# Kernel optimization log

Hardware: AMD Instinct MI355X
Metric: run time of the kernel (lower is better)

## Reference

```python
import jax, jax.numpy as jnp
from jax import lax
import numpy as np

H = 64
IN = 7
EPS = 1e-5


def _lstm_layer(x_seq, Wih, Whh, bih, bhh):
    # x_seq: [B, T, D] -> returns [B, T, H]; PyTorch gate order i,f,g,o
    B = x_seq.shape[0]
    b = bih + bhh
    x_tbd = jnp.swapaxes(x_seq, 0, 1)  # [T, B, D]
    # precompute input projections for all timesteps (one big GEMM)
    xproj = jnp.einsum('tbd,gd->tbg', x_tbd, Wih) + b  # [T, B, 4H]

    def step(carry, xp_t):
        h, c = carry
        gates = xp_t + h @ Whh.T  # [B, 4H]
        i, f, g, o = jnp.split(gates, 4, axis=-1)
        i = jax.nn.sigmoid(i)
        f = jax.nn.sigmoid(f)
        g = jnp.tanh(g)
        o = jax.nn.sigmoid(o)
        c = f * c + i * g
        h = o * jnp.tanh(c)
        return (h, c), h

    init = (jnp.zeros((B, H), x_seq.dtype), jnp.zeros((B, H), x_seq.dtype))
    _, hs = lax.scan(step, init, xproj)  # hs: [T, B, H]
    return jnp.swapaxes(hs, 0, 1)


def setup_inputs() -> dict:
    key = jax.random.key(0)
    ks = jax.random.split(key, 16)
    s = 1.0 / np.sqrt(H)
    u = lambda k, shape: jax.random.uniform(k, shape, jnp.float32, -s, s)
    inp = {
        'x': jax.random.normal(ks[0], (256, IN, 2048), jnp.float32),
        'Wih0': u(ks[1], (4 * H, IN)),
        'Whh0': u(ks[2], (4 * H, H)),
        'bih0': u(ks[3], (4 * H,)),
        'bhh0': u(ks[4], (4 * H,)),
        'Wih1': u(ks[5], (4 * H, H)),
        'Whh1': u(ks[6], (4 * H, H)),
        'bih1': u(ks[7], (4 * H,)),
        'bhh1': u(ks[8], (4 * H,)),
        'W1': u(ks[9], (10, H)),
        'b1': u(ks[10], (10,)),
        'gamma': jnp.ones((10,), jnp.float32),
        'beta': jnp.zeros((10,), jnp.float32),
        'rm': jax.random.normal(ks[11], (10,), jnp.float32) * 0.1,
        'rv': jax.random.uniform(ks[12], (10,), jnp.float32, 0.5, 1.5),
        'W2': u(ks[13], (1, 10)),
        'b2': u(ks[14], (1,)),
    }
    return inp


def reference(x, Wih0, Whh0, bih0, bhh0, Wih1, Whh1, bih1, bhh1,
              W1, b1, gamma, beta, rm, rv, W2, b2):
    # x: [B, 7, T] -> permute to [B, T, 7] (batch_first LSTM input)
    xs = jnp.transpose(x, (0, 2, 1))
    h0 = _lstm_layer(xs, Wih0, Whh0, bih0, bhh0)   # [B, T, H]
    h1 = _lstm_layer(h0, Wih1, Whh1, bih1, bhh1)   # [B, T, H] (dropout=0.05 inactive in eval)
    last = h1[:, -1, :]                            # [B, H]
    y = last @ W1.T + b1                           # [B, 10]
    y = (y - rm) * lax.rsqrt(rv + EPS) * gamma + beta  # BN1d eval mode
    y = jax.nn.relu(y)
    return y @ W2.T + b2                           # [B, 1]
```

## Files before the change

### kernel.cpp

```cpp
#include <hip/hip_runtime.h>
#include <math.h>

#define HH  64
#define TT  2048
#define IND 7
#define NT  256

typedef _Float16 half_t;
typedef _Float16 h2v __attribute__((ext_vector_type(2)));
typedef _Float16 h8v __attribute__((ext_vector_type(8)));
typedef unsigned int u2v __attribute__((ext_vector_type(2)));

#define LOG2E 1.44269504088896f

#define S2C(V, I) __builtin_shufflevector(V, V, 2*(I), 2*(I)+1)

__device__ __forceinline__ float fdot2(h2v a, h2v b, float c) {
#if __has_builtin(__builtin_amdgcn_fdot2)
    return __builtin_amdgcn_fdot2(a, b, c, false);
#else
    return fmaf((float)a.x, (float)b.x, fmaf((float)a.y, (float)b.y, c));
#endif
}

__device__ __forceinline__ float exp2_fast(float x) {
#if __has_builtin(__builtin_amdgcn_exp2f)
    return __builtin_amdgcn_exp2f(x);
#else
    return exp2f(x);
#endif
}
__device__ __forceinline__ float rcp_fast(float x) {
#if __has_builtin(__builtin_amdgcn_rcpf)
    return __builtin_amdgcn_rcpf(x);
#else
    return __fdividef(1.0f, x);
#endif
}

__device__ __forceinline__ float partner32(float x, int kh) {
#if __has_builtin(__builtin_amdgcn_permlane32_swap)
    u2v r = __builtin_amdgcn_permlane32_swap(__float_as_uint(x), __float_as_uint(x), false, false);
    return kh ? __uint_as_float(r.x) : __uint_as_float(r.y);
#else
    return __shfl_xor(x, 32);
#endif
}

__device__ __forceinline__ float sig2(float ahat) {
    return rcp_fast(1.0f + exp2_fast(-ahat));
}
__device__ __forceinline__ float tanh2(float c) {
    float e = exp2_fast(c * (-2.0f * LOG2E));
    return fmaf(2.0f, rcp_fast(1.0f + e), -1.0f);
}

#define DOT4(ACC, W, H) \
    ACC = fdot2((W)[0], S2C(H, 0), ACC); \
    ACC = fdot2((W)[1], S2C(H, 1), ACC); \
    ACC = fdot2((W)[2], S2C(H, 2), ACC); \
    ACC = fdot2((W)[3], S2C(H, 3), ACC);

__global__ __launch_bounds__(NT) __attribute__((amdgpu_waves_per_eu(1, 1)))
void lstm2_fused(
    const float* __restrict__ x,
    const float* __restrict__ Wih0,
    const float* __restrict__ Whh0,
    const float* __restrict__ bih0, const float* __restrict__ bhh0,
    const float* __restrict__ Wih1,
    const float* __restrict__ Whh1,
    const float* __restrict__ bih1, const float* __restrict__ bhh1,
    const float* __restrict__ W1,
    const float* __restrict__ b1v,
    const float* __restrict__ gmma, const float* __restrict__ beta,
    const float* __restrict__ rm,   const float* __restrict__ rv,
    const float* __restrict__ W2,
    const float* __restrict__ b2,
    float* __restrict__ out)
{
    const int b    = blockIdx.x;
    const int tid  = threadIdx.x;
    const int wave = tid >> 6;
    const int lane = tid & 63;
    const int kh   = lane >> 5;
    const int j    = ((wave & 1) << 5) | (lane & 31);
    const bool pub = (kh == 0);

    __shared__ __align__(16) half_t xTh[TT][8];
    __shared__ __align__(16) half_t h0r[4][HH];
    __shared__ __align__(16) half_t h1r[2][HH];
    __shared__ float yv[10];

    {
        const float* xg = x + (size_t)b * (IND * TT);
        for (int i = tid; i < IND * TT; i += NT) {
            int d = i >> 11;
            int t = i & (TT - 1);
            xTh[t][d] = (half_t)xg[i];
        }
        for (int t = tid; t < TT; t += NT) xTh[t][7] = (half_t)0.0f;
        if (tid < HH) {
            h0r[3][tid] = (half_t)0.0f;
            h1r[1][tid] = (half_t)0.0f;
        }
    }

    __syncthreads();

    if (wave < 2) {
        h2v wh[4][16];
        h2v xw[4][4];
        float bg[4];
        #pragma unroll
        for (int s = 0; s < 4; ++s) {
            const int g = (s << 6) | j;
            const float sc = (s == 2) ? 2.0f * LOG2E : LOG2E;
            const float* pw = Whh0 + g * HH + 32 * kh;
            #pragma unroll
            for (int r = 0; r < 16; ++r)
                wh[s][r] = h2v{(half_t)(pw[2*r] * sc), (half_t)(pw[2*r+1] * sc)};
            float t8[8];
            #pragma unroll
            for (int d = 0; d < 8; ++d)
                t8[d] = (d < IND && kh) ? Wih0[g * IND + d] * sc : 0.0f;
            #pragma unroll
            for (int r = 0; r < 4; ++r)
                xw[s][r] = h2v{(half_t)t8[2*r], (half_t)t8[2*r+1]};
            bg[s] = (kh == 0) ? (bih0[g] + bhh0[g]) * sc : 0.0f;
        }

        float c0 = 0.0f;
        h8v XV = *((const h8v*)&xTh[0][0]);

        for (int tick = 0; tick <= TT + 1; ++tick) {
            if (tick < TT) {
                const h8v* hp = (const h8v*)&h0r[(tick - 1) & 3][32 * kh];
                h8v H0 = hp[0], H1 = hp[1], H2 = hp[2], H3 = hp[3];
                float fr[4];
                #pragma unroll
                for (int s = 0; s < 4; ++s) {
                    float a0 = bg[s], a1 = 0.f, a2 = 0.f, a3 = 0.f;
                    DOT4(a0, &xw[s][0], XV)
                    DOT4(a0, &wh[s][0],  H0)
                    DOT4(a1, &wh[s][4],  H1)
                    DOT4(a2, &wh[s][8],  H2)
                    DOT4(a3, &wh[s][12], H3)
                    fr[s] = (a0 + a1) + (a2 + a3);
                }
                float fi = fr[0] + partner32(fr[0], kh);
                float ff = fr[1] + partner32(fr[1], kh);
                float fg = fr[2] + partner32(fr[2], kh);
                float fo = fr[3] + partner32(fr[3], kh);
                float iv = sig2(fi);
                float fv = sig2(ff);
                float gv = fmaf(2.0f, sig2(fg), -1.0f);
                float ov = sig2(fo);
                c0 = fmaf(fv, c0, iv * gv);
                float hn = ov * tanh2(c0);
                if (pub) h0r[tick & 3][j] = (half_t)hn;
                XV = *((const h8v*)&xTh[(tick + 1) & (TT - 1)][0]);
            }
            __syncthreads();
        }
    } else {
        h2v wi[4][16], wh[4][16];
        float bg[4];
        #pragma unroll
        for (int s = 0; s < 4; ++s) {
            const int g = (s << 6) | j;
            const float sc = (s == 2) ? 2.0f * LOG2E : LOG2E;
            const float* p0 = Wih1 + g * HH + 32 * kh;
            const float* p1 = Whh1 + g * HH + 32 * kh;
            #pragma unroll
            for (int r = 0; r < 16; ++r) {
                wi[s][r] = h2v{(half_t)(p0[2*r] * sc), (half_t)(p0[2*r+1] * sc)};
                wh[s][r] = h2v{(half_t)(p1[2*r] * sc), (half_t)(p1[2*r+1] * sc)};
            }
            bg[s] = (kh == 0) ? (bih1[g] + bhh1[g]) * sc : 0.0f;
        }

        float c1 = 0.0f;
        h8v P0 = {}, P1 = {}, P2 = {}, P3 = {};

        for (int tick = 0; tick <= TT + 1; ++tick) {
            if (tick >= 2) {
                const h8v* q = (const h8v*)&h1r[(tick - 3) & 1][32 * kh];
                h8v Q0 = q[0], Q1 = q[1], Q2 = q[2], Q3 = q[3];
                float fr[4];
                #pragma unroll
                for (int s = 0; s < 4; ++s) {
                    float a0 = bg[s], a1 = 0.f, a2 = 0.f, a3 = 0.f;
                    DOT4(a0, &wi[s][0],  P0)
                    DOT4(a1, &wi[s][4],  P1)
                    DOT4(a2, &wi[s][8],  P2)
                    DOT4(a3, &wi[s][12], P3)
                    DOT4(a0, &wh[s][0],  Q0)
                    DOT4(a1, &wh[s][4],  Q1)
                    DOT4(a2, &wh[s][8],  Q2)
                    DOT4(a3, &wh[s][12], Q3)
                    fr[s] = (a0 + a1) + (a2 + a3);
                }
                float fi = fr[0] + partner32(fr[0], kh);
                float ff = fr[1] + partner32(fr[1], kh);
                float fg = fr[2] + partner32(fr[2], kh);
                float fo = fr[3] + partner32(fr[3], kh);
                float iv = sig2(fi);
                float fv = sig2(ff);
                float gv = fmaf(2.0f, sig2(fg), -1.0f);
                float ov = sig2(fo);
                c1 = fmaf(fv, c1, iv * gv);
                float hn = ov * tanh2(c1);
                if (pub) h1r[tick & 1][j] = (half_t)hn;
            }
            if (tick >= 1) {
                const h8v* pp = (const h8v*)&h0r[(tick - 1) & 3][32 * kh];
                P0 = pp[0]; P1 = pp[1]; P2 = pp[2]; P3 = pp[3];
            }
            __syncthreads();
        }
    }

    if (tid < 10) {
        float y = b1v[tid];
        #pragma unroll
        for (int k = 0; k < HH; ++k) y += W1[tid * HH + k] * (float)h1r[1][k];
        y = (y - rm[tid]) * rsqrtf(rv[tid] + 1e-5f) * gmma[tid] + beta[tid];
        y = fmaxf(y, 0.0f);
        yv[tid] = y * W2[tid];
    }
    __syncthreads();
    if (tid == 0) {
        float sacc = b2[0];
        #pragma unroll
        for (int k = 0; k < 10; ++k) sacc += yv[k];
        out[b] = sacc;
    }
}

extern "C" void kernel_launch(void* const* d_in, const int* in_sizes, int n_in,
                              void* d_out, int out_size, void* d_ws, size_t ws_size,
                              hipStream_t stream) {
    const float* x    = (const float*)d_in[0];
    const float* Wih0 = (const float*)d_in[1];
    const float* Whh0 = (const float*)d_in[2];
    const float* bih0 = (const float*)d_in[3];
    const float* bhh0 = (const float*)d_in[4];
    const float* Wih1 = (const float*)d_in[5];
    const float* Whh1 = (const float*)d_in[6];
    const float* bih1 = (const float*)d_in[7];
    const float* bhh1 = (const float*)d_in[8];
    const float* W1   = (const float*)d_in[9];
    const float* b1   = (const float*)d_in[10];
    const float* gmma = (const float*)d_in[11];
    const float* beta = (const float*)d_in[12];
    const float* rm   = (const float*)d_in[13];
    const float* rv   = (const float*)d_in[14];
    const float* W2   = (const float*)d_in[15];
    const float* b2   = (const float*)d_in[16];

    const int B = in_sizes[0] / (IND * TT);

    lstm2_fused<<<dim3(B), dim3(NT), 0, stream>>>(
        x, Wih0, Whh0, bih0, bhh0, Wih1, Whh1, bih1, bhh1,
        W1, b1, gmma, beta, rm, rv, W2, b2, (float*)d_out);
}
```

Baseline: 1.040 ms.

## Offload LSTM input projections to dedicated producer waves via shared memory

Adds two more waves (384 threads) that compute the layer-0 input projection from x and the layer-1 input projection from layer-0 h. Both results go through double-buffered shared arrays, one tick ahead of the recurrent waves that consume them. The layer-0 and layer-1 recurrent waves then only do the hidden-to-hidden dot products on their serial per-timestep path, which halves layer-1 arithmetic per step. The cost is extra shared-memory traffic, a deeper pipeline and a barrier across six waves instead of four each step.

```diff
diff --git a/kernel.cpp b/kernel.cpp
--- a/kernel.cpp
+++ b/kernel.cpp
@@ -4,11 +4,12 @@
 #define HH  64
 #define TT  2048
 #define IND 7
-#define NT  256
+#define NT  384
 
 typedef _Float16 half_t;
 typedef _Float16 h2v __attribute__((ext_vector_type(2)));
 typedef _Float16 h8v __attribute__((ext_vector_type(8)));
+typedef float    f4v __attribute__((ext_vector_type(4)));
 typedef unsigned int u2v __attribute__((ext_vector_type(2)));
 
 #define LOG2E 1.44269504088896f
@@ -61,7 +62,7 @@
     ACC = fdot2((W)[2], S2C(H, 2), ACC); \
     ACC = fdot2((W)[3], S2C(H, 3), ACC);
 
-__global__ __launch_bounds__(NT) __attribute__((amdgpu_waves_per_eu(1, 1)))
+__global__ __launch_bounds__(NT) __attribute__((amdgpu_waves_per_eu(1, 2)))
 void lstm2_fused(
     const float* __restrict__ x,
     const float* __restrict__ Wih0,
@@ -89,6 +90,8 @@
     __shared__ __align__(16) half_t xTh[TT][8];
     __shared__ __align__(16) half_t h0r[4][HH];
     __shared__ __align__(16) half_t h1r[2][HH];
+    __shared__ __align__(16) float  zr[2][HH][2][4];
+    __shared__ __align__(16) float  xr[2][HH][2][4];
     __shared__ float yv[10];
 
     {
@@ -105,12 +108,8 @@
         }
     }
 
-    __syncthreads();
-
     if (wave < 2) {
         h2v wh[4][16];
-        h2v xw[4][4];
-        float bg[4];
         #pragma unroll
         for (int s = 0; s < 4; ++s) {
             const int g = (s << 6) | j;
@@ -119,28 +118,19 @@
             #pragma unroll
             for (int r = 0; r < 16; ++r)
                 wh[s][r] = h2v{(half_t)(pw[2*r] * sc), (half_t)(pw[2*r+1] * sc)};
-            float t8[8];
-            #pragma unroll
-            for (int d = 0; d < 8; ++d)
-                t8[d] = (d < IND && kh) ? Wih0[g * IND + d] * sc : 0.0f;
-            #pragma unroll
-            for (int r = 0; r < 4; ++r)
-                xw[s][r] = h2v{(half_t)t8[2*r], (half_t)t8[2*r+1]};
-            bg[s] = (kh == 0) ? (bih0[g] + bhh0[g]) * sc : 0.0f;
-        }
-
+        }
         float c0 = 0.0f;
-        h8v XV = *((const h8v*)&xTh[0][0]);
+        __syncthreads();
 
         for (int tick = 0; tick <= TT + 1; ++tick) {
             if (tick < TT) {
                 const h8v* hp = (const h8v*)&h0r[(tick - 1) & 3][32 * kh];
                 h8v H0 = hp[0], H1 = hp[1], H2 = hp[2], H3 = hp[3];
+                f4v xz = *((const f4v*)&xr[tick & 1][j][kh][0]);
                 float fr[4];
                 #pragma unroll
                 for (int s = 0; s < 4; ++s) {
-                    float a0 = bg[s], a1 = 0.f, a2 = 0.f, a3 = 0.f;
-                    DOT4(a0, &xw[s][0], XV)
+                    float a0 = xz[s], a1 = 0.f, a2 = 0.f, a3 = 0.f;
                     DOT4(a0, &wh[s][0],  H0)
                     DOT4(a1, &wh[s][4],  H1)
                     DOT4(a2, &wh[s][8],  H2)
@@ -158,42 +148,34 @@
                 c0 = fmaf(fv, c0, iv * gv);
                 float hn = ov * tanh2(c0);
                 if (pub) h0r[tick & 3][j] = (half_t)hn;
-                XV = *((const h8v*)&xTh[(tick + 1) & (TT - 1)][0]);
             }
             __syncthreads();
         }
-    } else {
-        h2v wi[4][16], wh[4][16];
+    } else if (wave < 4) {
+        h2v wh[4][16];
         float bg[4];
         #pragma unroll
         for (int s = 0; s < 4; ++s) {
             const int g = (s << 6) | j;
             const float sc = (s == 2) ? 2.0f * LOG2E : LOG2E;
-            const float* p0 = Wih1 + g * HH + 32 * kh;
-            const float* p1 = Whh1 + g * HH + 32 * kh;
-            #pragma unroll
-            for (int r = 0; r < 16; ++r) {
-                wi[s][r] = h2v{(half_t)(p0[2*r] * sc), (half_t)(p0[2*r+1] * sc)};
-                wh[s][r] = h2v{(half_t)(p1[2*r] * sc), (half_t)(p1[2*r+1] * sc)};
-            }
+            const float* pw = Whh1 + g * HH + 32 * kh;
+            #pragma unroll
+            for (int r = 0; r < 16; ++r)
+                wh[s][r] = h2v{(half_t)(pw[2*r] * sc), (half_t)(pw[2*r+1] * sc)};
             bg[s] = (kh == 0) ? (bih1[g] + bhh1[g]) * sc : 0.0f;
         }
-
         float c1 = 0.0f;
-        h8v P0 = {}, P1 = {}, P2 = {}, P3 = {};
+        __syncthreads();
 
         for (int tick = 0; tick <= TT + 1; ++tick) {
             if (tick >= 2) {
-                const h8v* q = (const h8v*)&h1r[(tick - 3) & 1][32 * kh];
-                h8v Q0 = q[0], Q1 = q[1], Q2 = q[2], Q3 = q[3];
+                const h8v* hq = (const h8v*)&h1r[(tick - 3) & 1][32 * kh];
+                h8v Q0 = hq[0], Q1 = hq[1], Q2 = hq[2], Q3 = hq[3];
+                f4v zv = *((const f4v*)&zr[(tick - 2) & 1][j][kh][0]);
                 float fr[4];
                 #pragma unroll
                 for (int s = 0; s < 4; ++s) {
-                    float a0 = bg[s], a1 = 0.f, a2 = 0.f, a3 = 0.f;
-                    DOT4(a0, &wi[s][0],  P0)
-                    DOT4(a1, &wi[s][4],  P1)
-                    DOT4(a2, &wi[s][8],  P2)
-                    DOT4(a3, &wi[s][12], P3)
+                    float a0 = bg[s] + zv[s], a1 = 0.f, a2 = 0.f, a3 = 0.f;
                     DOT4(a0, &wh[s][0],  Q0)
                     DOT4(a1, &wh[s][4],  Q1)
                     DOT4(a2, &wh[s][8],  Q2)
@@ -210,11 +192,77 @@
                 float ov = sig2(fo);
                 c1 = fmaf(fv, c1, iv * gv);
                 float hn = ov * tanh2(c1);
-                if (pub) h1r[tick & 1][j] = (half_t)hn;
-            }
-            if (tick >= 1) {
-                const h8v* pp = (const h8v*)&h0r[(tick - 1) & 3][32 * kh];
-                P0 = pp[0]; P1 = pp[1]; P2 = pp[2]; P3 = pp[3];
+                if (pub) h1r[(tick - 2) & 1][j] = (half_t)hn;
+            }
+            __syncthreads();
+        }
+    } else {
+        h2v wz[4][16];
+        h2v wx[4][4];
+        float bx[4];
+        #pragma unroll
+        for (int s = 0; s < 4; ++s) {
+            const int g = (s << 6) | j;
+            const float sc = (s == 2) ? 2.0f * LOG2E : LOG2E;
+            const float* pw = Wih1 + g * HH + 32 * kh;
+            #pragma unroll
+            for (int r = 0; r < 16; ++r)
+                wz[s][r] = h2v{(half_t)(pw[2*r] * sc), (half_t)(pw[2*r+1] * sc)};
+            float t8[8];
+            #pragma unroll
+            for (int d = 0; d < 8; ++d)
+                t8[d] = (d < IND && kh) ? Wih0[g * IND + d] * sc : 0.0f;
+            #pragma unroll
+            for (int r = 0; r < 4; ++r)
+                wx[s][r] = h2v{(half_t)t8[2*r], (half_t)t8[2*r+1]};
+            bx[s] = (kh == 0) ? (bih0[g] + bhh0[g]) * sc : 0.0f;
+        }
+        {
+            const float* xg = x + (size_t)b * (IND * TT);
+            #pragma unroll
+            for (int s = 0; s < 4; ++s) {
+                const int g = (s << 6) | j;
+                const float sc = (s == 2) ? 2.0f * LOG2E : LOG2E;
+                float acc;
+                if (kh) {
+                    acc = 0.0f;
+                    #pragma unroll
+                    for (int d = 0; d < IND; ++d) acc += Wih0[g * IND + d] * xg[d * TT];
+                    acc *= sc;
+                } else {
+                    acc = (bih0[g] + bhh0[g]) * sc;
+                }
+                xr[0][j][kh][s] = acc;
+            }
+        }
+        __syncthreads();
+
+        for (int tick = 0; tick <= TT + 1; ++tick) {
+            if (tick >= 1 && tick <= TT) {
+                const h8v* hp = (const h8v*)&h0r[(tick - 1) & 3][32 * kh];
+                h8v H0 = hp[0], H1 = hp[1], H2 = hp[2], H3 = hp[3];
+                float z[4];
+                #pragma unroll
+                for (int s = 0; s < 4; ++s) {
+                    float a0 = 0.f, a1 = 0.f, a2 = 0.f, a3 = 0.f;
+                    DOT4(a0, &wz[s][0],  H0)
+                    DOT4(a1, &wz[s][4],  H1)
+                    DOT4(a2, &wz[s][8],  H2)
+                    DOT4(a3, &wz[s][12], H3)
+                    z[s] = (a0 + a1) + (a2 + a3);
+                }
+                *((f4v*)&zr[(tick - 1) & 1][j][kh][0]) = f4v{z[0], z[1], z[2], z[3]};
+            }
+            if (tick + 1 < TT) {
+                h8v XV = *((const h8v*)&xTh[tick + 1][0]);
+                float xp[4];
+                #pragma unroll
+                for (int s = 0; s < 4; ++s) {
+                    float a = bx[s];
+                    DOT4(a, &wx[s][0], XV)
+                    xp[s] = a;
+                }
+                *((f4v*)&xr[(tick + 1) & 1][j][kh][0]) = f4v{xp[0], xp[1], xp[2], xp[3]};
             }
             __syncthreads();
         }
```

Measured after the change: 1.293 ms. 24.4% more time.

## Decouple LSTM layers with LDS ring buffer and spin-flag handshakes

Applied to the files above, without the earlier changes.

Shrinks the block to two waves, one per LSTM layer. Each lane now owns a full hidden unit, so the 64-wide dot products run inside the lane and the cross-half permlane reduction goes away. The per-tick block barrier is replaced by a 32-entry LDS ring of layer-0 outputs, with volatile progress counters that let layer 0 run ahead of layer 1. This removes lockstep barrier cost, but doubles per-lane register weights (layer 1 holds 256 h2v), which raises spill risk. It also relies on intra-wave write visibility before the next step's read without a barrier, since each wave reads its own previous h row.

```diff
diff --git a/kernel.cpp b/kernel.cpp
--- a/kernel.cpp
+++ b/kernel.cpp
@@ -4,12 +4,12 @@
 #define HH  64
 #define TT  2048
 #define IND 7
-#define NT  256
+#define NT  128
+#define RING 32
 
 typedef _Float16 half_t;
 typedef _Float16 h2v __attribute__((ext_vector_type(2)));
 typedef _Float16 h8v __attribute__((ext_vector_type(8)));
-typedef unsigned int u2v __attribute__((ext_vector_type(2)));
 
 #define LOG2E 1.44269504088896f
 
@@ -35,15 +35,6 @@
     return __builtin_amdgcn_rcpf(x);
 #else
     return __fdividef(1.0f, x);
-#endif
-}
-
-__device__ __forceinline__ float partner32(float x, int kh) {
-#if __has_builtin(__builtin_amdgcn_permlane32_swap)
-    u2v r = __builtin_amdgcn_permlane32_swap(__float_as_uint(x), __float_as_uint(x), false, false);
-    return kh ? __uint_as_float(r.x) : __uint_as_float(r.y);
-#else
-    return __shfl_xor(x, 32);
 #endif
 }
 
@@ -82,13 +73,11 @@
     const int tid  = threadIdx.x;
     const int wave = tid >> 6;
     const int lane = tid & 63;
-    const int kh   = lane >> 5;
-    const int j    = ((wave & 1) << 5) | (lane & 31);
-    const bool pub = (kh == 0);
 
     __shared__ __align__(16) half_t xTh[TT][8];
-    __shared__ __align__(16) half_t h0r[4][HH];
-    __shared__ __align__(16) half_t h1r[2][HH];
+    __shared__ __align__(16) half_t h0ring[RING][HH];
+    __shared__ __align__(16) half_t h1ring[2][HH];
+    __shared__ int progs[2];
     __shared__ float yv[10];
 
     {
@@ -100,130 +89,135 @@
         }
         for (int t = tid; t < TT; t += NT) xTh[t][7] = (half_t)0.0f;
         if (tid < HH) {
-            h0r[3][tid] = (half_t)0.0f;
-            h1r[1][tid] = (half_t)0.0f;
-        }
-    }
-
+            h0ring[RING - 1][tid] = (half_t)0.0f;
+            h1ring[1][tid]        = (half_t)0.0f;
+        }
+        if (tid == 0) { progs[0] = 0; progs[1] = 0; }
+    }
     __syncthreads();
 
-    if (wave < 2) {
-        h2v wh[4][16];
+    if (wave == 0) {
+        h2v wh[4][32];
         h2v xw[4][4];
         float bg[4];
         #pragma unroll
         for (int s = 0; s < 4; ++s) {
-            const int g = (s << 6) | j;
+            const int g = (s << 6) | lane;
             const float sc = (s == 2) ? 2.0f * LOG2E : LOG2E;
-            const float* pw = Whh0 + g * HH + 32 * kh;
-            #pragma unroll
-            for (int r = 0; r < 16; ++r)
+            const float* pw = Whh0 + g * HH;
+            #pragma unroll
+            for (int r = 0; r < 32; ++r)
                 wh[s][r] = h2v{(half_t)(pw[2*r] * sc), (half_t)(pw[2*r+1] * sc)};
             float t8[8];
             #pragma unroll
             for (int d = 0; d < 8; ++d)
-                t8[d] = (d < IND && kh) ? Wih0[g * IND + d] * sc : 0.0f;
+                t8[d] = (d < IND) ? Wih0[g * IND + d] * sc : 0.0f;
             #pragma unroll
             for (int r = 0; r < 4; ++r)
                 xw[s][r] = h2v{(half_t)t8[2*r], (half_t)t8[2*r+1]};
-            bg[s] = (kh == 0) ? (bih0[g] + bhh0[g]) * sc : 0.0f;
+            bg[s] = (bih0[g] + bhh0[g]) * sc;
         }
 
         float c0 = 0.0f;
-        h8v XV = *((const h8v*)&xTh[0][0]);
-
-        for (int tick = 0; tick <= TT + 1; ++tick) {
-            if (tick < TT) {
-                const h8v* hp = (const h8v*)&h0r[(tick - 1) & 3][32 * kh];
-                h8v H0 = hp[0], H1 = hp[1], H2 = hp[2], H3 = hp[3];
-                float fr[4];
-                #pragma unroll
-                for (int s = 0; s < 4; ++s) {
-                    float a0 = bg[s], a1 = 0.f, a2 = 0.f, a3 = 0.f;
-                    DOT4(a0, &xw[s][0], XV)
-                    DOT4(a0, &wh[s][0],  H0)
-                    DOT4(a1, &wh[s][4],  H1)
-                    DOT4(a2, &wh[s][8],  H2)
-                    DOT4(a3, &wh[s][12], H3)
-                    fr[s] = (a0 + a1) + (a2 + a3);
-                }
-                float fi = fr[0] + partner32(fr[0], kh);
-                float ff = fr[1] + partner32(fr[1], kh);
-                float fg = fr[2] + partner32(fr[2], kh);
-                float fo = fr[3] + partner32(fr[3], kh);
-                float iv = sig2(fi);
-                float fv = sig2(ff);
-                float gv = fmaf(2.0f, sig2(fg), -1.0f);
-                float ov = sig2(fo);
-                c0 = fmaf(fv, c0, iv * gv);
-                float hn = ov * tanh2(c0);
-                if (pub) h0r[tick & 3][j] = (half_t)hn;
-                XV = *((const h8v*)&xTh[(tick + 1) & (TT - 1)][0]);
-            }
-            __syncthreads();
+        for (int t = 0; t < TT; ++t) {
+            if (t >= RING) {
+                while (*(volatile int*)&progs[1] < t - (RING - 1)) { }
+            }
+            const h8v* hp = (const h8v*)&h0ring[(t - 1) & (RING - 1)][0];
+            h8v H0 = hp[0], H1 = hp[1], H2 = hp[2], H3 = hp[3];
+            h8v H4 = hp[4], H5 = hp[5], H6 = hp[6], H7 = hp[7];
+            h8v XV = *((const h8v*)&xTh[t][0]);
+            float fr[4];
+            #pragma unroll
+            for (int s = 0; s < 4; ++s) {
+                float a0 = bg[s], a1 = 0.f, a2 = 0.f, a3 = 0.f;
+                DOT4(a0, &wh[s][0],  H0)
+                DOT4(a1, &wh[s][4],  H1)
+                DOT4(a2, &wh[s][8],  H2)
+                DOT4(a3, &wh[s][12], H3)
+                DOT4(a0, &wh[s][16], H4)
+                DOT4(a1, &wh[s][20], H5)
+                DOT4(a2, &wh[s][24], H6)
+                DOT4(a3, &wh[s][28], H7)
+                DOT4(a0, &xw[s][0],  XV)
+                fr[s] = (a0 + a1) + (a2 + a3);
+            }
+            float iv = sig2(fr[0]);
+            float fv = sig2(fr[1]);
+            float gv = fmaf(2.0f, sig2(fr[2]), -1.0f);
+            float ov = sig2(fr[3]);
+            c0 = fmaf(fv, c0, iv * gv);
+            float hn = ov * tanh2(c0);
+            h0ring[t & (RING - 1)][lane] = (half_t)hn;
+            __threadfence_block();
+            if (lane == 0) *(volatile int*)&progs[0] = t + 1;
         }
     } else {
-        h2v wi[4][16], wh[4][16];
+        h2v wi[4][32], wr[4][32];
         float bg[4];
         #pragma unroll
         for (int s = 0; s < 4; ++s) {
-            const int g = (s << 6) | j;
+            const int g = (s << 6) | lane;
             const float sc = (s == 2) ? 2.0f * LOG2E : LOG2E;
-            const float* p0 = Wih1 + g * HH + 32 * kh;
-            const float* p1 = Whh1 + g * HH + 32 * kh;
-            #pragma unroll
-            for (int r = 0; r < 16; ++r) {
+            const float* p0 = Wih1 + g * HH;
+            const float* p1 = Whh1 + g * HH;
+            #pragma unroll
+            for (int r = 0; r < 32; ++r) {
                 wi[s][r] = h2v{(half_t)(p0[2*r] * sc), (half_t)(p0[2*r+1] * sc)};
-                wh[s][r] = h2v{(half_t)(p1[2*r] * sc), (half_t)(p1[2*r+1] * sc)};
-            }
-            bg[s] = (kh == 0) ? (bih1[g] + bhh1[g]) * sc : 0.0f;
+                wr[s][r] = h2v{(half_t)(p1[2*r] * sc), (half_t)(p1[2*r+1] * sc)};
+            }
+            bg[s] = (bih1[g] + bhh1[g]) * sc;
         }
 
         float c1 = 0.0f;
-        h8v P0 = {}, P1 = {}, P2 = {}, P3 = {};
-
-        for (int tick = 0; tick <= TT + 1; ++tick) {
-            if (tick >= 2) {
-                const h8v* q = (const h8v*)&h1r[(tick - 3) & 1][32 * kh];
-                h8v Q0 = q[0], Q1 = q[1], Q2 = q[2], Q3 = q[3];
-                float fr[4];
-                #pragma unroll
-                for (int s = 0; s < 4; ++s) {
-                    float a0 = bg[s], a1 = 0.f, a2 = 0.f, a3 = 0.f;
-                    DOT4(a0, &wi[s][0],  P0)
-                    DOT4(a1, &wi[s][4],  P1)
-                    DOT4(a2, &wi[s][8],  P2)
-                    DOT4(a3, &wi[s][12], P3)
-                    DOT4(a0, &wh[s][0],  Q0)
-                    DOT4(a1, &wh[s][4],  Q1)
-                    DOT4(a2, &wh[s][8],  Q2)
-                    DOT4(a3, &wh[s][12], Q3)
-                    fr[s] = (a0 + a1) + (a2 + a3);
-                }
-                float fi = fr[0] + partner32(fr[0], kh);
-                float ff = fr[1] + partner32(fr[1], kh);
-                float fg = fr[2] + partner32(fr[2], kh);
-                float fo = fr[3] + partner32(fr[3], kh);
-                float iv = sig2(fi);
-                float fv = sig2(ff);
-                float gv = fmaf(2.0f, sig2(fg), -1.0f);
-                float ov = sig2(fo);
-                c1 = fmaf(fv, c1, iv * gv);
-                float hn = ov * tanh2(c1);
-                if (pub) h1r[tick & 1][j] = (half_t)hn;
-            }
-            if (tick >= 1) {
-                const h8v* pp = (const h8v*)&h0r[(tick - 1) & 3][32 * kh];
-                P0 = pp[0]; P1 = pp[1]; P2 = pp[2]; P3 = pp[3];
-            }
-            __syncthreads();
-        }
-    }
+        for (int t = 0; t < TT; ++t) {
+            while (*(volatile int*)&progs[0] < t + 1) { }
+            const h8v* hp = (const h8v*)&h0ring[t & (RING - 1)][0];
+            h8v H0 = hp[0], H1 = hp[1], H2 = hp[2], H3 = hp[3];
+            h8v H4 = hp[4], H5 = hp[5], H6 = hp[6], H7 = hp[7];
+            const h8v* gq = (const h8v*)&h1ring[(t - 1) & 1][0];
+            h8v G0 = gq[0], G1 = gq[1], G2 = gq[2], G3 = gq[3];
+            h8v G4 = gq[4], G5 = gq[5], G6 = gq[6], G7 = gq[7];
+            __threadfence_block();
+            if (lane == 0) *(volatile int*)&progs[1] = t + 1;
+            float fr[4];
+            #pragma unroll
+            for (int s = 0; s < 4; ++s) {
+                float a0 = bg[s], a1 = 0.f, a2 = 0.f, a3 = 0.f;
+                DOT4(a0, &wi[s][0],  H0)
+                DOT4(a1, &wi[s][4],  H1)
+                DOT4(a2, &wi[s][8],  H2)
+                DOT4(a3, &wi[s][12], H3)
+                DOT4(a0, &wi[s][16], H4)
+                DOT4(a1, &wi[s][20], H5)
+                DOT4(a2, &wi[s][24], H6)
+                DOT4(a3, &wi[s][28], H7)
+                DOT4(a0, &wr[s][0],  G0)
+                DOT4(a1, &wr[s][4],  G1)
+                DOT4(a2, &wr[s][8],  G2)
+                DOT4(a3, &wr[s][12], G3)
+                DOT4(a0, &wr[s][16], G4)
+                DOT4(a1, &wr[s][20], G5)
+                DOT4(a2, &wr[s][24], G6)
+                DOT4(a3, &wr[s][28], G7)
+                fr[s] = (a0 + a1) + (a2 + a3);
+            }
+            float iv = sig2(fr[0]);
+            float fv = sig2(fr[1]);
+            float gv = fmaf(2.0f, sig2(fr[2]), -1.0f);
+            float ov = sig2(fr[3]);
+            c1 = fmaf(fv, c1, iv * gv);
+            float hn = ov * tanh2(c1);
+            h1ring[t & 1][lane] = (half_t)hn;
+        }
+    }
+
+    __syncthreads();
 
     if (tid < 10) {
         float y = b1v[tid];
         #pragma unroll
-        for (int k = 0; k < HH; ++k) y += W1[tid * HH + k] * (float)h1r[1][k];
+        for (int k = 0; k < HH; ++k) y += W1[tid * HH + k] * (float)h1ring[1][k];
         y = (y - rm[tid]) * rsqrtf(rv[tid] + 1e-5f) * gmma[tid] + beta[tid];
         y = fmaxf(y, 0.0f);
         yv[tid] = y * W2[tid];
```

Measured after the change: 1.797 ms. 1.73x slower.

## Rebalance LSTM work between wave groups by moving projections across layers

Applied to the files above, without the earlier changes.

Layer-0 waves now also compute the layer-1 input projection Wih1·h0 and pass it through shared memory. Layer-1 waves take over the layer-0 input projection Wih0·x one step ahead through a double-buffered xr array. This evens out the per-tick dot-product load between the two wave groups, since the layer-1 waves previously did twice the work on each barrier step. The cost is extra shared-memory traffic for fp32 partial sums, a different pipeline skew, and higher register use from holding wz weights.

```diff
diff --git a/kernel.cpp b/kernel.cpp
--- a/kernel.cpp
+++ b/kernel.cpp
@@ -9,6 +9,7 @@
 typedef _Float16 half_t;
 typedef _Float16 h2v __attribute__((ext_vector_type(2)));
 typedef _Float16 h8v __attribute__((ext_vector_type(8)));
+typedef float    f4v __attribute__((ext_vector_type(4)));
 typedef unsigned int u2v __attribute__((ext_vector_type(2)));
 
 #define LOG2E 1.44269504088896f
@@ -87,8 +88,10 @@
     const bool pub = (kh == 0);
 
     __shared__ __align__(16) half_t xTh[TT][8];
-    __shared__ __align__(16) half_t h0r[4][HH];
+    __shared__ __align__(16) half_t h0r[2][HH];
     __shared__ __align__(16) half_t h1r[2][HH];
+    __shared__ __align__(16) float  zr[2][2][HH][4];
+    __shared__ __align__(16) float  xr[2][HH][4];
     __shared__ float yv[10];
 
     {
@@ -100,104 +103,121 @@
         }
         for (int t = tid; t < TT; t += NT) xTh[t][7] = (half_t)0.0f;
         if (tid < HH) {
-            h0r[3][tid] = (half_t)0.0f;
+            h0r[1][tid] = (half_t)0.0f;
             h1r[1][tid] = (half_t)0.0f;
-        }
-    }
-
+            #pragma unroll
+            for (int s = 0; s < 4; ++s) {
+                const int g = (s << 6) | tid;
+                const float sc = (s == 2) ? 2.0f * LOG2E : LOG2E;
+                float acc = bih0[g] + bhh0[g];
+                #pragma unroll
+                for (int d = 0; d < IND; ++d) acc += Wih0[g * IND + d] * xg[d * TT];
+                xr[0][tid][s] = acc * sc;
+            }
+        }
+    }
     __syncthreads();
 
     if (wave < 2) {
-        h2v wh[4][16];
-        h2v xw[4][4];
-        float bg[4];
+        h2v wh[4][16], wz[4][16];
         #pragma unroll
         for (int s = 0; s < 4; ++s) {
             const int g = (s << 6) | j;
             const float sc = (s == 2) ? 2.0f * LOG2E : LOG2E;
             const float* pw = Whh0 + g * HH + 32 * kh;
+            const float* pz = Wih1 + g * HH + 32 * kh;
+            #pragma unroll
+            for (int r = 0; r < 16; ++r) {
+                wh[s][r] = h2v{(half_t)(pw[2*r] * sc), (half_t)(pw[2*r+1] * sc)};
+                wz[s][r] = h2v{(half_t)(pz[2*r] * sc), (half_t)(pz[2*r+1] * sc)};
+            }
+        }
+        float c0 = 0.0f;
+
+        for (int T = 0; T <= TT + 1; ++T) {
+            if (T <= TT) {
+                const h8v* hp = (const h8v*)&h0r[(T - 1) & 1][32 * kh];
+                h8v H0 = hp[0], H1 = hp[1], H2 = hp[2], H3 = hp[3];
+                if (T < TT) {
+                    f4v xp = *((const f4v*)&xr[T & 1][j][0]);
+                    float fr[4];
+                    #pragma unroll
+                    for (int s = 0; s < 4; ++s) {
+                        float a0 = pub ? xp[s] : 0.0f;
+                        float a1 = 0.f, a2 = 0.f, a3 = 0.f;
+                        DOT4(a0, &wh[s][0],  H0)
+                        DOT4(a1, &wh[s][4],  H1)
+                        DOT4(a2, &wh[s][8],  H2)
+                        DOT4(a3, &wh[s][12], H3)
+                        fr[s] = (a0 + a1) + (a2 + a3);
+                    }
+                    float fi = fr[0] + partner32(fr[0], kh);
+                    float ff = fr[1] + partner32(fr[1], kh);
+                    float fg = fr[2] + partner32(fr[2], kh);
+                    float fo = fr[3] + partner32(fr[3], kh);
+                    float iv = sig2(fi);
+                    float fv = sig2(ff);
+                    float gv = fmaf(2.0f, sig2(fg), -1.0f);
+                    float ov = sig2(fo);
+                    c0 = fmaf(fv, c0, iv * gv);
+                    float hn = ov * tanh2(c0);
+                    if (pub) h0r[T & 1][j] = (half_t)hn;
+                }
+                if (T >= 1) {
+                    float za[4];
+                    #pragma unroll
+                    for (int s = 0; s < 4; ++s) {
+                        float a0 = 0.f, a1 = 0.f, a2 = 0.f, a3 = 0.f;
+                        DOT4(a0, &wz[s][0],  H0)
+                        DOT4(a1, &wz[s][4],  H1)
+                        DOT4(a2, &wz[s][8],  H2)
+                        DOT4(a3, &wz[s][12], H3)
+                        za[s] = (a0 + a1) + (a2 + a3);
+                    }
+                    *((f4v*)&zr[(T - 1) & 1][kh][j][0]) = f4v{za[0], za[1], za[2], za[3]};
+                }
+            }
+            __syncthreads();
+        }
+    } else {
+        h2v wr[4][16], wx[4][4];
+        float bg1[4], bx0[4];
+        #pragma unroll
+        for (int s = 0; s < 4; ++s) {
+            const int g = (s << 6) | j;
+            const float sc = (s == 2) ? 2.0f * LOG2E : LOG2E;
+            const float* pw = Whh1 + g * HH + 32 * kh;
             #pragma unroll
             for (int r = 0; r < 16; ++r)
-                wh[s][r] = h2v{(half_t)(pw[2*r] * sc), (half_t)(pw[2*r+1] * sc)};
+                wr[s][r] = h2v{(half_t)(pw[2*r] * sc), (half_t)(pw[2*r+1] * sc)};
             float t8[8];
             #pragma unroll
             for (int d = 0; d < 8; ++d)
-                t8[d] = (d < IND && kh) ? Wih0[g * IND + d] * sc : 0.0f;
+                t8[d] = (d < IND) ? Wih0[g * IND + d] * sc : 0.0f;
             #pragma unroll
             for (int r = 0; r < 4; ++r)
-                xw[s][r] = h2v{(half_t)t8[2*r], (half_t)t8[2*r+1]};
-            bg[s] = (kh == 0) ? (bih0[g] + bhh0[g]) * sc : 0.0f;
-        }
-
-        float c0 = 0.0f;
-        h8v XV = *((const h8v*)&xTh[0][0]);
-
-        for (int tick = 0; tick <= TT + 1; ++tick) {
-            if (tick < TT) {
-                const h8v* hp = (const h8v*)&h0r[(tick - 1) & 3][32 * kh];
-                h8v H0 = hp[0], H1 = hp[1], H2 = hp[2], H3 = hp[3];
+                wx[s][r] = h2v{(half_t)t8[2*r], (half_t)t8[2*r+1]};
+            bg1[s] = (bih1[g] + bhh1[g]) * sc;
+            bx0[s] = (bih0[g] + bhh0[g]) * sc;
+        }
+        float c1 = 0.0f;
+
+        for (int T = 0; T <= TT + 1; ++T) {
+            if (T >= 2) {
+                const h8v* hq = (const h8v*)&h1r[(T - 3) & 1][32 * kh];
+                h8v Q0 = hq[0], Q1 = hq[1], Q2 = hq[2], Q3 = hq[3];
+                f4v za = *((const f4v*)&zr[(T - 2) & 1][0][j][0]);
+                f4v zb = *((const f4v*)&zr[(T - 2) & 1][1][j][0]);
+                f4v zs = za + zb;
                 float fr[4];
                 #pragma unroll
                 for (int s = 0; s < 4; ++s) {
-                    float a0 = bg[s], a1 = 0.f, a2 = 0.f, a3 = 0.f;
-                    DOT4(a0, &xw[s][0], XV)
-                    DOT4(a0, &wh[s][0],  H0)
-                    DOT4(a1, &wh[s][4],  H1)
-                    DOT4(a2, &wh[s][8],  H2)
-                    DOT4(a3, &wh[s][12], H3)
-                    fr[s] = (a0 + a1) + (a2 + a3);
-                }
-                float fi = fr[0] + partner32(fr[0], kh);
-                float ff = fr[1] + partner32(fr[1], kh);
-                float fg = fr[2] + partner32(fr[2], kh);
-                float fo = fr[3] + partner32(fr[3], kh);
-                float iv = sig2(fi);
-                float fv = sig2(ff);
-                float gv = fmaf(2.0f, sig2(fg), -1.0f);
-                float ov = sig2(fo);
-                c0 = fmaf(fv, c0, iv * gv);
-                float hn = ov * tanh2(c0);
-                if (pub) h0r[tick & 3][j] = (half_t)hn;
-                XV = *((const h8v*)&xTh[(tick + 1) & (TT - 1)][0]);
-            }
-            __syncthreads();
-        }
-    } else {
-        h2v wi[4][16], wh[4][16];
-        float bg[4];
-        #pragma unroll
-        for (int s = 0; s < 4; ++s) {
-            const int g = (s << 6) | j;
-            const float sc = (s == 2) ? 2.0f * LOG2E : LOG2E;
-            const float* p0 = Wih1 + g * HH + 32 * kh;
-            const float* p1 = Whh1 + g * HH + 32 * kh;
-            #pragma unroll
-            for (int r = 0; r < 16; ++r) {
-                wi[s][r] = h2v{(half_t)(p0[2*r] * sc), (half_t)(p0[2*r+1] * sc)};
-                wh[s][r] = h2v{(half_t)(p1[2*r] * sc), (half_t)(p1[2*r+1] * sc)};
-            }
-            bg[s] = (kh == 0) ? (bih1[g] + bhh1[g]) * sc : 0.0f;
-        }
-
-        float c1 = 0.0f;
-        h8v P0 = {}, P1 = {}, P2 = {}, P3 = {};
-
-        for (int tick = 0; tick <= TT + 1; ++tick) {
-            if (tick >= 2) {
-                const h8v* q = (const h8v*)&h1r[(tick - 3) & 1][32 * kh];
-                h8v Q0 = q[0], Q1 = q[1], Q2 = q[2], Q3 = q[3];
-                float fr[4];
-                #pragma unroll
-                for (int s = 0; s < 4; ++s) {
-                    float a0 = bg[s], a1 = 0.f, a2 = 0.f, a3 = 0.f;
-                    DOT4(a0, &wi[s][0],  P0)
-                    DOT4(a1, &wi[s][4],  P1)
-                    DOT4(a2, &wi[s][8],  P2)
-                    DOT4(a3, &wi[s][12], P3)
-                    DOT4(a0, &wh[s][0],  Q0)
-                    DOT4(a1, &wh[s][4],  Q1)
-                    DOT4(a2, &wh[s][8],  Q2)
-                    DOT4(a3, &wh[s][12], Q3)
+                    float a0 = pub ? (bg1[s] + zs[s]) : 0.0f;
+                    float a1 = 0.f, a2 = 0.f, a3 = 0.f;
+                    DOT4(a0, &wr[s][0],  Q0)
+                    DOT4(a1, &wr[s][4],  Q1)
+                    DOT4(a2, &wr[s][8],  Q2)
+                    DOT4(a3, &wr[s][12], Q3)
                     fr[s] = (a0 + a1) + (a2 + a3);
                 }
                 float fi = fr[0] + partner32(fr[0], kh);
@@ -210,11 +230,18 @@
                 float ov = sig2(fo);
                 c1 = fmaf(fv, c1, iv * gv);
                 float hn = ov * tanh2(c1);
-                if (pub) h1r[tick & 1][j] = (half_t)hn;
-            }
-            if (tick >= 1) {
-                const h8v* pp = (const h8v*)&h0r[(tick - 1) & 3][32 * kh];
-                P0 = pp[0]; P1 = pp[1]; P2 = pp[2]; P3 = pp[3];
+                if (pub) h1r[(T - 2) & 1][j] = (half_t)hn;
+            }
+            if (T + 1 < TT) {
+                h8v XV = *((const h8v*)&xTh[T + 1][0]);
+                float xp[4];
+                #pragma unroll
+                for (int s = 0; s < 4; ++s) {
+                    float a = bx0[s];
+                    DOT4(a, &wx[s][0], XV)
+                    xp[s] = a;
+                }
+                if (pub) *((f4v*)&xr[(T + 1) & 1][j][0]) = f4v{xp[0], xp[1], xp[2], xp[3]};
             }
             __syncthreads();
         }
```

After: 1.208 ms. +16.2%, slower.
